# Kernel optimization log

Hardware: AMD Instinct MI355X
Metric: run time of the kernel (lower is better)

Reference implementation:

```python
import jax, jax.numpy as jnp
import numpy as np
from jax.scipy.special import logsumexp

N_STATES = 512
N_OBS = 1024
BATCH = 64
T_MAX = 512


def setup_inputs() -> dict:
    key = jax.random.key(0)
    k1, k2, k3, k4, k5 = jax.random.split(key, 5)
    pi = jnp.zeros((N_STATES,), dtype=jnp.float32)
    A = jax.random.normal(k1, (N_STATES, N_STATES), dtype=jnp.float32)  # unnormalized transition
    E = jax.random.normal(k2, (N_STATES, N_OBS), dtype=jnp.float32)     # unnormalized emission
    x = jax.random.randint(k3, (BATCH, T_MAX), 0, N_OBS)
    T = jax.random.randint(k4, (BATCH,), 1, T_MAX + 1)
    return {"pi": pi, "A": A, "E": E, "x": x, "T": T}


def reference(pi, A, E, x, T):
    # log p(x) via forward algorithm in log domain.
    log_pi = jax.nn.log_softmax(pi)                # (N,)
    log_A = jax.nn.log_softmax(A, axis=0)          # (N,N), matches torch dim=0
    log_E = jax.nn.log_softmax(E, axis=1)          # (N,M)

    # emission log-probs per timestep: (B, T_max, N)
    log_em = jnp.moveaxis(log_E[:, x], 0, -1)

    alpha0 = log_em[:, 0, :] + log_pi              # (B,N)

    def step(carry, em_t):
        # carry: (B,N) over k; log_A: (N_i, N_k)
        # next[b,i] = em_t[b,i] + logsumexp_k(log_A[i,k] + carry[b,k])
        nxt = em_t + logsumexp(log_A[None, :, :] + carry[:, None, :], axis=2)
        return nxt, nxt

    em_rest = jnp.swapaxes(log_em[:, 1:, :], 0, 1)  # (T_max-1, B, N)
    _, alphas = jax.lax.scan(step, alpha0, em_rest)
    log_alpha = jnp.concatenate([alpha0[:, None, :], jnp.swapaxes(alphas, 0, 1)], axis=1)  # (B,T_max,N)

    log_sums = logsumexp(log_alpha, axis=2)         # (B, T_max)
    log_probs = jnp.take_along_axis(log_sums, (T - 1)[:, None], axis=1)  # (B,1)
    return log_probs
```

## Files before the change

kernel.cpp:

```cpp
#include <hip/hip_runtime.h>
#include <math.h>

#define NS   512
#define NO   1024
#define NB   64
#define TMAX 512

#define QREG 45
#define QLDS 19

typedef _Float16 h2v __attribute__((ext_vector_type(2)));

__device__ inline float wave_red_sum(float x) {
#pragma unroll
  for (int o = 32; o; o >>= 1) x += __shfl_xor(x, o, 64);
  return x;
}
__device__ inline float wave_red_max(float x) {
#pragma unroll
  for (int o = 32; o; o >>= 1) x = fmaxf(x, __shfl_xor(x, o, 64));
  return x;
}

__device__ inline float dot2u(unsigned int a, unsigned int b, float c) {
#if __has_builtin(__builtin_amdgcn_fdot2)
  return __builtin_amdgcn_fdot2(__builtin_bit_cast(h2v, a),
                                __builtin_bit_cast(h2v, b), c, false);
#else
  h2v av = __builtin_bit_cast(h2v, a), bv = __builtin_bit_cast(h2v, b);
  return c + (float)av.x * (float)bv.x + (float)av.y * (float)bv.y;
#endif
}

__global__ void k_pi(const float* __restrict__ pi, float* __restrict__ pi_sm) {
  __shared__ float red[8];
  int tid = threadIdx.x;
  float v = pi[tid];
  float m = wave_red_max(v);
  if ((tid & 63) == 0) red[tid >> 6] = m;
  __syncthreads();
  m = fmaxf(fmaxf(fmaxf(red[0], red[1]), fmaxf(red[2], red[3])),
            fmaxf(fmaxf(red[4], red[5]), fmaxf(red[6], red[7])));
  float e = __expf(v - m);
  float s = wave_red_sum(e);
  __syncthreads();
  if ((tid & 63) == 0) red[tid >> 6] = s;
  __syncthreads();
  s = red[0] + red[1] + red[2] + red[3] + red[4] + red[5] + red[6] + red[7];
  pi_sm[tid] = e / s;
}

__global__ void k_colLse(const float* __restrict__ A, float* __restrict__ lseA) {
  __shared__ float redm[4];
  __shared__ float reds[4];
  int k = blockIdx.x, tid = threadIdx.x;
  float a0 = A[tid * NS + k], a1 = A[(tid + 256) * NS + k];
  float m = wave_red_max(fmaxf(a0, a1));
  if ((tid & 63) == 0) redm[tid >> 6] = m;
  __syncthreads();
  m = fmaxf(fmaxf(redm[0], redm[1]), fmaxf(redm[2], redm[3]));
  float s = __expf(a0 - m) + __expf(a1 - m);
  s = wave_red_sum(s);
  if ((tid & 63) == 0) reds[tid >> 6] = s;
  __syncthreads();
  s = reds[0] + reds[1] + reds[2] + reds[3];
  if (tid == 0) lseA[k] = m + __logf(s);
}

__global__ void k_rowLseE(const float* __restrict__ E, float* __restrict__ lseE) {
  __shared__ float red[4];
  int i = blockIdx.x, tid = threadIdx.x;
  const float* row = E + i * NO;
  float a0 = row[tid], a1 = row[tid + 256], a2 = row[tid + 512], a3 = row[tid + 768];
  float m = fmaxf(fmaxf(a0, a1), fmaxf(a2, a3));
  m = wave_red_max(m);
  if ((tid & 63) == 0) red[tid >> 6] = m;
  __syncthreads();
  m = fmaxf(fmaxf(red[0], red[1]), fmaxf(red[2], red[3]));
  float s = __expf(a0 - m) + __expf(a1 - m) + __expf(a2 - m) + __expf(a3 - m);
  s = wave_red_sum(s);
  __syncthreads();
  if ((tid & 63) == 0) red[tid >> 6] = s;
  __syncthreads();
  s = red[0] + red[1] + red[2] + red[3];
  if (tid == 0) lseE[i] = m + __logf(s);
}

__global__ void k_pack(const float* __restrict__ A, const float* __restrict__ lseA,
                       unsigned int* __restrict__ W) {
  int u = blockIdx.x * 512 + threadIdx.x;
  int q = u >> 11;
  int r = u & 2047;
  int i = r >> 2;
  int h = r & 3;
  int k0 = q * 8 + h * 2;
  float e0 = __expf(A[i * NS + k0]     - lseA[k0]);
  float e1 = __expf(A[i * NS + k0 + 1] - lseA[k0 + 1]);
  h2v p;
  p.x = (_Float16)e0;
  p.y = (_Float16)e1;
  W[u] = __builtin_bit_cast(unsigned int, p);
}

__global__ __launch_bounds__(512, 1) void k_fwd(
    const float* __restrict__ E, const int* __restrict__ x,
    const int* __restrict__ Tlen, const float* __restrict__ pi_sm,
    const float* __restrict__ lseE, const uint4* __restrict__ Aall,
    float* __restrict__ out) {
  __shared__ uint4 Alds[QLDS * 512];
  __shared__ uint4 vbuf[2][NS / 8];
  __shared__ int xrow[TMAX];
  __shared__ __align__(16) float red[2][8];
  int b = blockIdx.x, tid = threadIdx.x;

  uint4 areg[QREG];
#pragma unroll
  for (int q = 0; q < QREG; q++) areg[q] = Aall[q * 512 + tid];
#pragma unroll
  for (int q = 0; q < QLDS; q++) Alds[q * 512 + tid] = Aall[(QREG + q) * 512 + tid];

  for (int t = tid; t < TMAX; t += 512) xrow[t] = x[b * TMAX + t];

  float pi_i  = pi_sm[tid];
  float lse_i = lseE[tid];
  const float* Erow = E + tid * NO;
  int Tb = Tlen[b];
  float c = 0.f;
  float Dlog = 0.f;
  int gexp_prev = 19;
  int cur = 0;
  __syncthreads();

  for (int t = 0; t < Tb; t++) {
    int nxt = cur ^ 1;
    float epre = Erow[xrow[t]];
    int gexpw;
    if (t == 0) {
      gexpw = 19;
    } else {
      const float4* rp = (const float4*)red[cur];
      float4 ra = rp[0], rb = rp[1];
      float sp = ((ra.x + ra.y) + (ra.z + ra.w)) + ((rb.x + rb.y) + (rb.z + rb.w));
      float ls = __log2f(sp);
      int e = ((__builtin_bit_cast(int, sp) >> 23) & 0xff) - 126;
      c += ls - Dlog;
      Dlog = (float)gexp_prev + ls;
      gexpw = 19 - gexp_prev - e;
    }
    float acc;
    if (t == 0) {
      acc = pi_i;
    } else {
      float a0 = 0.f, a1 = 0.f, a2 = 0.f, a3 = 0.f;
      const uint4* vp = vbuf[cur];
#pragma unroll
      for (int q = 0; q < QREG; q++) {
        uint4 vv = vp[q];
        a0 = dot2u(areg[q].x, vv.x, a0);
        a1 = dot2u(areg[q].y, vv.y, a1);
        a2 = dot2u(areg[q].z, vv.z, a2);
        a3 = dot2u(areg[q].w, vv.w, a3);
      }
#pragma unroll
      for (int q = 0; q < QLDS; q++) {
        uint4 av = Alds[q * 512 + tid];
        uint4 vv = vp[QREG + q];
        a0 = dot2u(av.x, vv.x, a0);
        a1 = dot2u(av.y, vv.y, a1);
        a2 = dot2u(av.z, vv.z, a2);
        a3 = dot2u(av.w, vv.w, a3);
      }
      acc = (a0 + a1) + (a2 + a3);
    }
    float em = __expf(epre - lse_i);
    float raw = acc * em;
    ((_Float16*)vbuf[nxt])[tid] = (_Float16)ldexpf(raw, gexpw);
    float s = wave_red_sum(raw);
    if ((tid & 63) == 0) red[nxt][tid >> 6] = s;
    gexp_prev = gexpw;
    cur = nxt;
    __syncthreads();
  }
  {
    const float4* rp = (const float4*)red[cur];
    float4 ra = rp[0], rb = rp[1];
    float sp = ((ra.x + ra.y) + (ra.z + ra.w)) + ((rb.x + rb.y) + (rb.z + rb.w));
    c += __log2f(sp) - Dlog;
  }
  if (tid == 0) out[b] = c * 0.69314718055994530942f;
}

extern "C" void kernel_launch(void* const* d_in, const int* in_sizes, int n_in,
                              void* d_out, int out_size, void* d_ws, size_t ws_size,
                              hipStream_t stream) {
  const float* pi = (const float*)d_in[0];
  const float* A  = (const float*)d_in[1];
  const float* E  = (const float*)d_in[2];
  const int*   x  = (const int*)d_in[3];
  const int*   T  = (const int*)d_in[4];
  float* out = (float*)d_out;

  char* ws = (char*)d_ws;
  float*        pi_sm = (float*)(ws + 0);
  float*        lseA  = (float*)(ws + 2048);
  float*        lseE  = (float*)(ws + 4096);
  unsigned int* Apk   = (unsigned int*)(ws + 6144);

  hipLaunchKernelGGL(k_pi,      dim3(1),   dim3(512), 0, stream, pi, pi_sm);
  hipLaunchKernelGGL(k_colLse,  dim3(512), dim3(256), 0, stream, A, lseA);
  hipLaunchKernelGGL(k_rowLseE, dim3(512), dim3(256), 0, stream, E, lseE);
  hipLaunchKernelGGL(k_pack,    dim3(256), dim3(512), 0, stream, A, lseA, Apk);
  hipLaunchKernelGGL(k_fwd,     dim3(64),  dim3(512), 0, stream,
                     E, x, T, pi_sm, lseE, (const uint4*)Apk, out);
}
```

Measured before the change: 919.0 us.

## Store transition matrix as FP8 E5M2 and expand to fp16 for dot2

```diff
diff --git a/kernel.cpp b/kernel.cpp
--- a/kernel.cpp
+++ b/kernel.cpp
@@ -6,8 +6,8 @@
 #define NB   64
 #define TMAX 512
 
-#define QREG 45
-#define QLDS 19
+#define QREG 22
+#define QLDS 10
 
 typedef _Float16 h2v __attribute__((ext_vector_type(2)));
 
@@ -32,6 +32,27 @@
 #endif
 }
 
+__device__ inline unsigned int ex_lo(unsigned int w) {
+#if __has_builtin(__builtin_amdgcn_perm)
+  return __builtin_amdgcn_perm(0u, w, 0x010C000Cu);
+#else
+  return ((w & 0xFFu) << 8) | ((w & 0xFF00u) << 16);
+#endif
+}
+__device__ inline unsigned int ex_hi(unsigned int w) {
+#if __has_builtin(__builtin_amdgcn_perm)
+  return __builtin_amdgcn_perm(0u, w, 0x030C020Cu);
+#else
+  return ((w & 0x00FF0000u) >> 8) | (w & 0xFF000000u);
+#endif
+}
+
+__device__ inline unsigned int f2e5m2(float f) {
+  unsigned short hb = __builtin_bit_cast(unsigned short, (_Float16)f);
+  unsigned int r = (unsigned int)hb + 0x7Fu + ((hb >> 8) & 1u);
+  return (r >> 8) & 0xFFu;
+}
+
 __global__ void k_pi(const float* __restrict__ pi, float* __restrict__ pi_sm) {
   __shared__ float red[8];
   int tid = threadIdx.x;
@@ -89,17 +110,17 @@
 __global__ void k_pack(const float* __restrict__ A, const float* __restrict__ lseA,
                        unsigned int* __restrict__ W) {
   int u = blockIdx.x * 512 + threadIdx.x;
-  int q = u >> 11;
-  int r = u & 2047;
-  int i = r >> 2;
-  int h = r & 3;
-  int k0 = q * 8 + h * 2;
-  float e0 = __expf(A[i * NS + k0]     - lseA[k0]);
-  float e1 = __expf(A[i * NS + k0 + 1] - lseA[k0 + 1]);
-  h2v p;
-  p.x = (_Float16)e0;
-  p.y = (_Float16)e1;
-  W[u] = __builtin_bit_cast(unsigned int, p);
+  int h = u & 3;
+  int qi = u >> 2;
+  int i = qi & 511;
+  int q = qi >> 9;
+  int k0 = q * 16 + h * 4;
+  const float* row = A + i * NS;
+  unsigned int b0 = f2e5m2(__expf(row[k0]     - lseA[k0])     * 256.f);
+  unsigned int b1 = f2e5m2(__expf(row[k0 + 1] - lseA[k0 + 1]) * 256.f);
+  unsigned int b2 = f2e5m2(__expf(row[k0 + 2] - lseA[k0 + 2]) * 256.f);
+  unsigned int b3 = f2e5m2(__expf(row[k0 + 3] - lseA[k0 + 3]) * 256.f);
+  W[u] = b0 | (b1 << 8) | (b2 << 16) | (b3 << 24);
 }
 
 __global__ __launch_bounds__(512, 1) void k_fwd(
@@ -155,22 +176,34 @@
       const uint4* vp = vbuf[cur];
 #pragma unroll
       for (int q = 0; q < QREG; q++) {
-        uint4 vv = vp[q];
-        a0 = dot2u(areg[q].x, vv.x, a0);
-        a1 = dot2u(areg[q].y, vv.y, a1);
-        a2 = dot2u(areg[q].z, vv.z, a2);
-        a3 = dot2u(areg[q].w, vv.w, a3);
+        uint4 av = areg[q];
+        uint4 va = vp[2 * q];
+        uint4 vb = vp[2 * q + 1];
+        a0 = dot2u(ex_lo(av.x), va.x, a0);
+        a0 = dot2u(ex_hi(av.x), va.y, a0);
+        a1 = dot2u(ex_lo(av.y), va.z, a1);
+        a1 = dot2u(ex_hi(av.y), va.w, a1);
+        a2 = dot2u(ex_lo(av.z), vb.x, a2);
+        a2 = dot2u(ex_hi(av.z), vb.y, a2);
+        a3 = dot2u(ex_lo(av.w), vb.z, a3);
+        a3 = dot2u(ex_hi(av.w), vb.w, a3);
       }
 #pragma unroll
       for (int q = 0; q < QLDS; q++) {
         uint4 av = Alds[q * 512 + tid];
-        uint4 vv = vp[QREG + q];
-        a0 = dot2u(av.x, vv.x, a0);
-        a1 = dot2u(av.y, vv.y, a1);
-        a2 = dot2u(av.z, vv.z, a2);
-        a3 = dot2u(av.w, vv.w, a3);
+        int cq = QREG + q;
+        uint4 va = vp[2 * cq];
+        uint4 vb = vp[2 * cq + 1];
+        a0 = dot2u(ex_lo(av.x), va.x, a0);
+        a0 = dot2u(ex_hi(av.x), va.y, a0);
+        a1 = dot2u(ex_lo(av.y), va.z, a1);
+        a1 = dot2u(ex_hi(av.y), va.w, a1);
+        a2 = dot2u(ex_lo(av.z), vb.x, a2);
+        a2 = dot2u(ex_hi(av.z), vb.y, a2);
+        a3 = dot2u(ex_lo(av.w), vb.z, a3);
+        a3 = dot2u(ex_hi(av.w), vb.w, a3);
       }
-      acc = (a0 + a1) + (a2 + a3);
+      acc = ((a0 + a1) + (a2 + a3)) * 0.00390625f;
     }
     float em = __expf(epre - lse_i);
     float raw = acc * em;
@@ -209,7 +242,7 @@
   hipLaunchKernelGGL(k_pi,      dim3(1),   dim3(512), 0, stream, pi, pi_sm);
   hipLaunchKernelGGL(k_colLse,  dim3(512), dim3(256), 0, stream, A, lseA);
   hipLaunchKernelGGL(k_rowLseE, dim3(512), dim3(256), 0, stream, E, lseE);
-  hipLaunchKernelGGL(k_pack,    dim3(256), dim3(512), 0, stream, A, lseA, Apk);
+  hipLaunchKernelGGL(k_pack,    dim3(128), dim3(512), 0, stream, A, lseA, Apk);
   hipLaunchKernelGGL(k_fwd,     dim3(64),  dim3(512), 0, stream,
                      E, x, T, pi_sm, lseE, (const uint4*)Apk, out);
 }
```

Result: slower. 1.263 ms (+37.4%).

## Repartition matvec so each wave covers a k-slice, reducing partials through LDS

Applied to the files above, without the earlier changes.

```diff
diff --git a/kernel.cpp b/kernel.cpp
--- a/kernel.cpp
+++ b/kernel.cpp
@@ -6,8 +6,8 @@
 #define NB   64
 #define TMAX 512
 
-#define QREG 45
-#define QLDS 19
+#define QREG 48
+#define QLDS 16
 
 typedef _Float16 h2v __attribute__((ext_vector_type(2)));
 
@@ -89,11 +89,14 @@
 __global__ void k_pack(const float* __restrict__ A, const float* __restrict__ lseA,
                        unsigned int* __restrict__ W) {
   int u = blockIdx.x * 512 + threadIdx.x;
-  int q = u >> 11;
-  int r = u & 2047;
-  int i = r >> 2;
-  int h = r & 3;
-  int k0 = q * 8 + h * 2;
+  int h = u & 3;
+  int ct = u >> 2;
+  int t = ct & 511;
+  int c = ct >> 9;
+  int j = c >> 3, m = c & 7;
+  int w = t >> 6, l = t & 63;
+  int i  = 64 * j + l;
+  int k0 = 64 * w + 8 * m + 2 * h;
   float e0 = __expf(A[i * NS + k0]     - lseA[k0]);
   float e1 = __expf(A[i * NS + k0 + 1] - lseA[k0 + 1]);
   h2v p;
@@ -105,21 +108,23 @@
 __global__ __launch_bounds__(512, 1) void k_fwd(
     const float* __restrict__ E, const int* __restrict__ x,
     const int* __restrict__ Tlen, const float* __restrict__ pi_sm,
-    const float* __restrict__ lseE, const uint4* __restrict__ Aall,
+    const float* __restrict__ lseE, const uint4* __restrict__ Apk,
     float* __restrict__ out) {
   __shared__ uint4 Alds[QLDS * 512];
+  __shared__ float Pf[8 * 512];
   __shared__ uint4 vbuf[2][NS / 8];
   __shared__ int xrow[TMAX];
   __shared__ __align__(16) float red[2][8];
   int b = blockIdx.x, tid = threadIdx.x;
+  int w = tid >> 6, l = tid & 63;
 
   uint4 areg[QREG];
 #pragma unroll
-  for (int q = 0; q < QREG; q++) areg[q] = Aall[q * 512 + tid];
-#pragma unroll
-  for (int q = 0; q < QLDS; q++) Alds[q * 512 + tid] = Aall[(QREG + q) * 512 + tid];
-
-  for (int t = tid; t < TMAX; t += 512) xrow[t] = x[b * TMAX + t];
+  for (int q = 0; q < QREG; q++) areg[q] = Apk[q * 512 + tid];
+#pragma unroll
+  for (int q = 0; q < QLDS; q++) Alds[q * 512 + tid] = Apk[(QREG + q) * 512 + tid];
+
+  for (int t2 = tid; t2 < TMAX; t2 += 512) xrow[t2] = x[b * TMAX + t2];
 
   float pi_i  = pi_sm[tid];
   float lse_i = lseE[tid];
@@ -147,39 +152,54 @@
       Dlog = (float)gexp_prev + ls;
       gexpw = 19 - gexp_prev - e;
     }
-    float acc;
-    if (t == 0) {
-      acc = pi_i;
-    } else {
-      float a0 = 0.f, a1 = 0.f, a2 = 0.f, a3 = 0.f;
+    if (t) {
       const uint4* vp = vbuf[cur];
-#pragma unroll
-      for (int q = 0; q < QREG; q++) {
-        uint4 vv = vp[q];
-        a0 = dot2u(areg[q].x, vv.x, a0);
-        a1 = dot2u(areg[q].y, vv.y, a1);
-        a2 = dot2u(areg[q].z, vv.z, a2);
-        a3 = dot2u(areg[q].w, vv.w, a3);
+      uint4 uv0 = vp[8 * w + 0], uv1 = vp[8 * w + 1];
+      uint4 uv2 = vp[8 * w + 2], uv3 = vp[8 * w + 3];
+      uint4 uv4 = vp[8 * w + 4], uv5 = vp[8 * w + 5];
+      uint4 uv6 = vp[8 * w + 6], uv7 = vp[8 * w + 7];
+      float acc[8];
+#pragma unroll
+      for (int j = 0; j < 8; j++) acc[j] = 0.f;
+#pragma unroll
+      for (int j = 0; j < 8; j++) {
+#pragma unroll
+        for (int m = 0; m < 8; m++) {
+          int cq = j * 8 + m;
+          uint4 av = (cq < QREG) ? areg[cq] : Alds[(cq - QREG) * 512 + tid];
+          uint4 uv = (m == 0) ? uv0 : (m == 1) ? uv1 : (m == 2) ? uv2 :
+                     (m == 3) ? uv3 : (m == 4) ? uv4 : (m == 5) ? uv5 :
+                     (m == 6) ? uv6 : uv7;
+          acc[j] = dot2u(av.x, uv.x, acc[j]);
+          acc[j] = dot2u(av.y, uv.y, acc[j]);
+          acc[j] = dot2u(av.z, uv.z, acc[j]);
+          acc[j] = dot2u(av.w, uv.w, acc[j]);
+        }
       }
 #pragma unroll
-      for (int q = 0; q < QLDS; q++) {
-        uint4 av = Alds[q * 512 + tid];
-        uint4 vv = vp[QREG + q];
-        a0 = dot2u(av.x, vv.x, a0);
-        a1 = dot2u(av.y, vv.y, a1);
-        a2 = dot2u(av.z, vv.z, a2);
-        a3 = dot2u(av.w, vv.w, a3);
+      for (int j = 0; j < 8; j++) Pf[w * 512 + j * 64 + l] = acc[j];
+    }
+    __syncthreads();
+
+    {
+      float em = __expf(epre - lse_i);
+      float raw;
+      if (t) {
+        float s0 = Pf[tid]          + Pf[512 + tid];
+        float s1 = Pf[1024 + tid]   + Pf[1536 + tid];
+        float s2 = Pf[2048 + tid]   + Pf[2560 + tid];
+        float s3 = Pf[3072 + tid]   + Pf[3584 + tid];
+        raw = ((s0 + s1) + (s2 + s3)) * em;
+      } else {
+        raw = pi_i * em;
       }
-      acc = (a0 + a1) + (a2 + a3);
+      ((_Float16*)vbuf[nxt])[tid] = (_Float16)ldexpf(raw, gexpw);
+      float s = wave_red_sum(raw);
+      if (l == 0) red[nxt][w] = s;
+      gexp_prev = gexpw;
     }
-    float em = __expf(epre - lse_i);
-    float raw = acc * em;
-    ((_Float16*)vbuf[nxt])[tid] = (_Float16)ldexpf(raw, gexpw);
-    float s = wave_red_sum(raw);
-    if ((tid & 63) == 0) red[nxt][tid >> 6] = s;
-    gexp_prev = gexpw;
+    __syncthreads();
     cur = nxt;
-    __syncthreads();
   }
   {
     const float4* rp = (const float4*)red[cur];
```

Result: faster. 886.5 us (-3.5%).
